# Performance work log

Hardware: AMD Instinct MI355X
Metric: run time of the kernel (lower is better)

## Reference

```python
import jax, jax.numpy as jnp
import numpy as np

E = 8          # num experts
TOPK = 2
D = 1024       # emb_size (expert hidden == emb_size)


def setup_inputs() -> dict:
    key = jax.random.key(0)
    ks = jax.random.split(key, 8)
    s = 1.0 / np.sqrt(D)
    x = jax.random.normal(ks[0], (4, 1024, D), dtype=jnp.float32)
    gate_W = jax.random.uniform(ks[1], (E, D), jnp.float32, -s, s)   # torch Linear weight (out,in)
    gate_b = jax.random.uniform(ks[2], (E,), jnp.float32, -s, s)
    w1 = jax.random.uniform(ks[3], (E, D, D), jnp.float32, -s, s)    # per-expert first Linear (out,in)
    b1 = jax.random.uniform(ks[4], (E, D), jnp.float32, -s, s)
    w2 = jax.random.uniform(ks[5], (E, D, D), jnp.float32, -s, s)    # per-expert second Linear (out,in)
    b2 = jax.random.uniform(ks[6], (E, D), jnp.float32, -s, s)
    return {"x": x, "gate_W": gate_W, "gate_b": gate_b,
            "w1": w1, "b1": b1, "w2": w2, "b2": b2}


def reference(x, gate_W, gate_b, w1, b1, w2, b2):
    x_shape = x.shape
    xt = x.reshape(-1, x_shape[-1])                       # [N, D]

    # gating
    gate_logits = xt @ gate_W.T + gate_b                  # [N, E]
    gate_prob = jax.nn.softmax(gate_logits, axis=-1)      # [N, E]
    top_w, top_i = jax.lax.top_k(gate_prob, TOPK)         # [N, K]
    top_w = jax.nn.softmax(top_w, axis=-1)                # renormalize over top-k

    # dense per-expert MLP: h = relu(x @ W1^T + b1); o = h @ W2^T + b2
    h = jax.nn.relu(jnp.einsum('nd,ehd->neh', xt, w1) + b1[None])   # [N, E, D]
    o = jnp.einsum('neh,eoh->neo', h, w2) + b2[None]                # [N, E, D]

    # gather top-k expert outputs per token and combine with weights
    o_top = jnp.take_along_axis(o, top_i[:, :, None], axis=1)       # [N, K, D]
    y = jnp.sum(o_top * top_w[:, :, None], axis=1)                  # [N, D]

    return y.reshape(x_shape), gate_prob
```

## Files before the change

kernel.cpp:

```cpp
#include <hip/hip_runtime.h>

#define NTOK 4096
#define DIM 1024
#define NE 8
#define NPAIR (NTOK * 2)

typedef __bf16 bf16x8 __attribute__((ext_vector_type(8)));
typedef float floatx4 __attribute__((ext_vector_type(4)));

__device__ __forceinline__ unsigned short f2bf(float f) {
  unsigned u = __float_as_uint(f);
  u = u + 0x7fffu + ((u >> 16) & 1u);
  return (unsigned short)(u >> 16);
}
__device__ __forceinline__ float bf2f(unsigned short h) {
  return __uint_as_float(((unsigned)h) << 16);
}

__device__ __forceinline__ void gld_lds16(const unsigned short* g, unsigned short* l) {
  __builtin_amdgcn_global_load_lds(
      (const __attribute__((address_space(1))) void*)g,
      (__attribute__((address_space(3))) void*)l, 16, 0, 0);
}

__global__ __launch_bounds__(256) void gate_kernel(
    const float* __restrict__ x, const float* __restrict__ gW,
    const float* __restrict__ gb,
    float* __restrict__ gp_out, int2* __restrict__ tops,
    float* __restrict__ pairw, int* __restrict__ cnt, int* __restrict__ done,
    unsigned short* __restrict__ x_bf)
{
  const int tid = threadIdx.x;
  if (blockIdx.x == 0) {
    if (tid < NE) cnt[tid] = 0;
    if (tid == NE) *done = 0;
  }
  const int lane = tid & 63;
  const int wid = tid >> 6;
  const int t = blockIdx.x * 4 + wid;

  float4 xv[4];
#pragma unroll
  for (int j = 0; j < 4; j++)
    xv[j] = ((const float4*)(x + (size_t)t * DIM))[lane + 64 * j];

#pragma unroll
  for (int j = 0; j < 4; j++) {
    ushort4 o;
    o.x = f2bf(xv[j].x); o.y = f2bf(xv[j].y);
    o.z = f2bf(xv[j].z); o.w = f2bf(xv[j].w);
    ((ushort4*)(x_bf + (size_t)t * DIM))[lane + 64 * j] = o;
  }

  float p[NE];
#pragma unroll
  for (int e = 0; e < NE; e++) {
    const float4* gwe = (const float4*)(gW + e * DIM);
    float s = 0.f;
#pragma unroll
    for (int j = 0; j < 4; j++) {
      float4 g = gwe[lane + 64 * j];
      s += xv[j].x * g.x + xv[j].y * g.y + xv[j].z * g.z + xv[j].w * g.w;
    }
    p[e] = s;
  }
#pragma unroll
  for (int e = 0; e < NE; e++) {
#pragma unroll
    for (int off = 32; off >= 1; off >>= 1) p[e] += __shfl_xor(p[e], off);
  }

  float m = -1e30f;
#pragma unroll
  for (int e = 0; e < NE; e++) { p[e] += gb[e]; m = fmaxf(m, p[e]); }
  float s = 0.f;
  float pr[NE];
#pragma unroll
  for (int e = 0; e < NE; e++) { pr[e] = __expf(p[e] - m); s += pr[e]; }
  float inv = 1.f / s;
#pragma unroll
  for (int e = 0; e < NE; e++) pr[e] *= inv;

  if (lane < NE) gp_out[(size_t)t * NE + lane] = pr[lane];

  if (lane == 0) {
    int i0 = 0;
#pragma unroll
    for (int e = 1; e < NE; e++) if (pr[e] > pr[i0]) i0 = e;
    int i1 = (i0 == 0) ? 1 : 0;
#pragma unroll
    for (int e = 0; e < NE; e++) if (e != i0 && pr[e] > pr[i1]) i1 = e;
    float d = __expf(pr[i1] - pr[i0]);
    float w0 = 1.f / (1.f + d);
    tops[t] = make_int2(i0, i1);
    pairw[t * 2] = w0;
    pairw[t * 2 + 1] = 1.f - w0;
  }
}

__global__ __launch_bounds__(256) void bin_sched_kernel(
    const int2* __restrict__ tops, int* __restrict__ cnt,
    int* __restrict__ bucket,
    int* __restrict__ posmap,
    int* __restrict__ done, int* __restrict__ base,
    int* __restrict__ sched, int* __restrict__ sched_n)
{
  const int t = blockIdx.x * 256 + threadIdx.x;
  const int lane = threadIdx.x & 63;
  int2 ti = tops[t];
#pragma unroll
  for (int slot = 0; slot < 2; slot++) {
    int e = slot ? ti.y : ti.x;
#pragma unroll
    for (int ex = 0; ex < NE; ex++) {
      bool mine = (e == ex);
      unsigned long long mask = __ballot(mine);
      if (mask) {
        int leader = __ffsll((long long)mask) - 1;
        int total = __popcll(mask);
        int prefix = __popcll(mask & ((1ull << lane) - 1ull));
        int idx = 0;
        if (lane == leader) idx = atomicAdd(&cnt[ex], total);
        idx = __shfl(idx, leader) + prefix;
        if (mine) {
          bucket[ex * NTOK + idx] = t * 2 + slot;
          posmap[t * 2 + slot] = (ex << 16) | idx;
        }
      }
    }
  }
  __syncthreads();
  if (threadIdx.x == 0) {
    if (atomicAdd(done, 1) == gridDim.x - 1) {
      int b = 0, pos = 0;
      for (int e = 0; e < NE; e++) {
        int c = atomicAdd(&cnt[e], 0);
        base[e] = b;
        int tiles = (c + 127) >> 7;
        for (int i = 0; i < tiles; i++) {
          int valid = c - i * 128; if (valid > 128) valid = 128;
          sched[pos++] = (e << 20) | (i << 8) | valid;
        }
        b += c;
      }
      base[NE] = b;
      *sched_n = pos;
    }
  }
}

__global__ __launch_bounds__(256) void cvt_kernel(
    const float4* __restrict__ src, ushort4* __restrict__ dst)
{
  const int i = blockIdx.x * 256 + threadIdx.x;
  float4 v = src[i];
  ushort4 o;
  o.x = f2bf(v.x); o.y = f2bf(v.y); o.z = f2bf(v.z); o.w = f2bf(v.w);
  dst[i] = o;
}

template <int RELU, int GATHER>
__global__ __launch_bounds__(256) void ffn_gemm(
    const unsigned short* __restrict__ A,
    const unsigned short* __restrict__ B,
    const float* __restrict__ bias,
    const int* __restrict__ base,
    const int* __restrict__ bucket,
    const int* __restrict__ sched, const int* __restrict__ sched_n,
    unsigned short* __restrict__ Out)
{
  const int l = blockIdx.x;
  const int xcd = l & 7;
  const int w = l >> 3;
  const int nt = w & 7;
  const int slot = xcd * 9 + (w >> 3);
  if (slot >= *sched_n) return;
  const int se = sched[slot];
  const int e = se >> 20;
  const int mt = (se >> 8) & 0xfff;
  const int valid = se & 255;
  const int arow0 = base[e] + mt * 128;

  __shared__ unsigned short lda[2][128 * 64];
  __shared__ unsigned short ldb[2][128 * 64];

  const int tid = threadIdx.x;
  const int lane = tid & 63;
  const int wid = tid >> 6;

  const unsigned short* ap[4];
  const unsigned short* bp[4];
#pragma unroll
  for (int j = 0; j < 4; j++) {
    int g = wid * 4 + j;
    int row = g * 8 + (lane >> 3);
    int gran = (lane & 7) ^ (row & 7);
    if (GATHER) {
      int idx = mt * 128 + row;
      int ce = base[e + 1] - base[e];
      if (idx > ce - 1) idx = ce - 1;
      int tok = bucket[e * NTOK + idx] >> 1;
      ap[j] = A + (size_t)tok * DIM + (gran << 3);
    } else {
      int prow = arow0 + row;
      if (prow > NPAIR - 1) prow = NPAIR - 1;
      ap[j] = A + (size_t)prow * DIM + (gran << 3);
    }
    bp[j] = B + ((size_t)e * DIM + nt * 128 + row) * DIM + (gran << 3);
  }

  floatx4 acc[4][4] = {};
  const int wm = (wid & 1) * 64;
  const int wn = (wid >> 1) * 64;
  const int quad = lane >> 4;
  const int cl = lane & 15;
  const int sw = cl & 7;

  auto stage = [&](int b) {
#pragma unroll
    for (int j = 0; j < 4; j++) {
      int g = wid * 4 + j;
      gld_lds16(ap[j], &lda[b][g * 512]);
      gld_lds16(bp[j], &ldb[b][g * 512]);
      ap[j] += 64;
      bp[j] += 64;
    }
  };
  auto compute = [&](int b) {
    const unsigned short* la = lda[b];
    const unsigned short* lb = ldb[b];
#pragma unroll
    for (int kk = 0; kk < 64; kk += 32) {
      const int gb = (kk >> 3) + quad;
      const int goff = ((gb ^ sw) << 3);
      bf16x8 af[4], bfr[4];
#pragma unroll
      for (int mi = 0; mi < 4; mi++)
        af[mi] = *(const bf16x8*)&la[(wm + mi * 16 + cl) * 64 + goff];
#pragma unroll
      for (int ni = 0; ni < 4; ni++)
        bfr[ni] = *(const bf16x8*)&lb[(wn + ni * 16 + cl) * 64 + goff];
#pragma unroll
      for (int mi = 0; mi < 4; mi++)
#pragma unroll
        for (int ni = 0; ni < 4; ni++)
          acc[mi][ni] = __builtin_amdgcn_mfma_f32_16x16x32_bf16(af[mi], bfr[ni], acc[mi][ni], 0, 0, 0);
    }
  };

  stage(0);
  asm volatile("s_waitcnt vmcnt(0)" ::: "memory");
  __builtin_amdgcn_s_barrier();

#pragma unroll 1
  for (int i = 0; i < 7; i++) {
    stage(1);
    compute(0);
    asm volatile("s_waitcnt vmcnt(0)" ::: "memory");
    __builtin_amdgcn_s_barrier();
    stage(0);
    compute(1);
    asm volatile("s_waitcnt vmcnt(0)" ::: "memory");
    __builtin_amdgcn_s_barrier();
  }
  stage(1);
  compute(0);
  asm volatile("s_waitcnt vmcnt(0)" ::: "memory");
  __builtin_amdgcn_s_barrier();
  compute(1);

#pragma unroll
  for (int ni = 0; ni < 4; ni++) {
    int col = nt * 128 + wn + ni * 16 + cl;
    float bval = bias[e * DIM + col];
#pragma unroll
    for (int mi = 0; mi < 4; mi++) {
#pragma unroll
      for (int reg = 0; reg < 4; reg++) {
        int rl = wm + mi * 16 + quad * 4 + reg;
        if (rl < valid) {
          float v = acc[mi][ni][reg] + bval;
          if (RELU) v = fmaxf(v, 0.f);
          Out[(size_t)(arow0 + rl) * DIM + col] = f2bf(v);
        }
      }
    }
  }
}

__global__ __launch_bounds__(256) void combine_kernel(
    const unsigned short* __restrict__ o, const int* __restrict__ posmap,
    const int* __restrict__ base, const float* __restrict__ pairw,
    float* __restrict__ y)
{
  const int t = blockIdx.x;
  const int tid = threadIdx.x;
  const int pm0 = posmap[t * 2], pm1 = posmap[t * 2 + 1];
  const int p0 = base[pm0 >> 16] + (pm0 & 0xffff);
  const int p1 = base[pm1 >> 16] + (pm1 & 0xffff);
  const float w0 = pairw[t * 2], w1 = pairw[t * 2 + 1];
  ushort4 a = ((const ushort4*)(o + (size_t)p0 * DIM))[tid];
  ushort4 b = ((const ushort4*)(o + (size_t)p1 * DIM))[tid];
  float4 r;
  r.x = w0 * bf2f(a.x) + w1 * bf2f(b.x);
  r.y = w0 * bf2f(a.y) + w1 * bf2f(b.y);
  r.z = w0 * bf2f(a.z) + w1 * bf2f(b.z);
  r.w = w0 * bf2f(a.w) + w1 * bf2f(b.w);
  ((float4*)(y + (size_t)t * DIM))[tid] = r;
}

extern "C" void kernel_launch(void* const* d_in, const int* in_sizes, int n_in,
                              void* d_out, int out_size, void* d_ws, size_t ws_size,
                              hipStream_t stream) {
  const float* x  = (const float*)d_in[0];
  const float* gW = (const float*)d_in[1];
  const float* gb = (const float*)d_in[2];
  const float* w1 = (const float*)d_in[3];
  const float* b1 = (const float*)d_in[4];
  const float* w2 = (const float*)d_in[5];
  const float* b2 = (const float*)d_in[6];
  float* y  = (float*)d_out;
  float* gp = (float*)d_out + (size_t)NTOK * DIM;

  char* ws = (char*)d_ws;
  unsigned short* x_bf   = (unsigned short*)(ws);
  unsigned short* w2_bf  = (unsigned short*)(ws);
  unsigned short* h_pack = (unsigned short*)(ws + (size_t)(16u << 20));
  unsigned short* w1_bf  = (unsigned short*)(ws + (size_t)(32u << 20));
  unsigned short* o_pack = (unsigned short*)(ws + (size_t)(32u << 20));
  char* tail = ws + (size_t)(48u << 20);
  int*   cnt     = (int*)(tail);
  int*   done    = cnt + NE;
  int*   base    = done + 1;
  int*   sched   = base + NE + 1;
  int*   sched_n = sched + 128;
  int*   bucket  = sched_n + 1;
  float* pairw   = (float*)(bucket + NE * NTOK);
  int2*  tops    = (int2*)(pairw + NPAIR);
  int*   posmap  = (int*)(tops + NTOK);

  const int cvt_blocks = (NE * DIM * DIM / 4) / 256;
  gate_kernel<<<NTOK / 4, 256, 0, stream>>>(x, gW, gb, gp, tops, pairw, cnt, done, x_bf);
  bin_sched_kernel<<<NTOK / 256, 256, 0, stream>>>(tops, cnt, bucket, posmap, done,
                                                   base, sched, sched_n);
  cvt_kernel<<<cvt_blocks, 256, 0, stream>>>((const float4*)w1, (ushort4*)w1_bf);
  ffn_gemm<1, 1><<<576, 256, 0, stream>>>(x_bf, w1_bf, b1, base, bucket, sched, sched_n, h_pack);
  cvt_kernel<<<cvt_blocks, 256, 0, stream>>>((const float4*)w2, (ushort4*)w2_bf);
  ffn_gemm<0, 0><<<576, 256, 0, stream>>>(h_pack, w2_bf, b2, base, bucket, sched, sched_n, o_pack);
  combine_kernel<<<NTOK, 256, 0, stream>>>(o_pack, posmap, base, pairw, y);
}
```

Before: 264.0 us.

## Halve expert GEMM M-tile to 64 rows and use single-buffered LDS

The expert schedule now uses 64-row token tiles instead of 128, and the grid grows so that 17 slots per XCD cover the larger tile count. Each of the four waves now handles a 64x32 slice of output. The double-buffered LDS staging is replaced by a single buffer with a barrier on each K step. The aim is better load balance across CUs for uneven expert sizes and higher occupancy from the smaller LDS footprint. In exchange, loads no longer overlap compute, and each block re-reads the full weight tile for fewer rows, which doubles weight traffic per token.

```diff
diff --git a/kernel.cpp b/kernel.cpp
--- a/kernel.cpp
+++ b/kernel.cpp
@@ -4,6 +4,7 @@
 #define DIM 1024
 #define NE 8
 #define NPAIR (NTOK * 2)
+#define NSLOT 17
 
 typedef __bf16 bf16x8 __attribute__((ext_vector_type(8)));
 typedef float floatx4 __attribute__((ext_vector_type(4)));
@@ -136,9 +137,9 @@
       for (int e = 0; e < NE; e++) {
         int c = atomicAdd(&cnt[e], 0);
         base[e] = b;
-        int tiles = (c + 127) >> 7;
+        int tiles = (c + 63) >> 6;
         for (int i = 0; i < tiles; i++) {
-          int valid = c - i * 128; if (valid > 128) valid = 128;
+          int valid = c - i * 64; if (valid > 64) valid = 64;
           sched[pos++] = (e << 20) | (i << 8) | valid;
         }
         b += c;
@@ -173,30 +174,30 @@
   const int xcd = l & 7;
   const int w = l >> 3;
   const int nt = w & 7;
-  const int slot = xcd * 9 + (w >> 3);
+  const int slot = xcd * NSLOT + (w >> 3);
   if (slot >= *sched_n) return;
   const int se = sched[slot];
   const int e = se >> 20;
   const int mt = (se >> 8) & 0xfff;
   const int valid = se & 255;
-  const int arow0 = base[e] + mt * 128;
-
-  __shared__ unsigned short lda[2][128 * 64];
-  __shared__ unsigned short ldb[2][128 * 64];
+  const int arow0 = base[e] + mt * 64;
+
+  __shared__ unsigned short lda[64 * 64];
+  __shared__ unsigned short ldb[128 * 64];
 
   const int tid = threadIdx.x;
   const int lane = tid & 63;
   const int wid = tid >> 6;
 
-  const unsigned short* ap[4];
+  const unsigned short* ap[2];
   const unsigned short* bp[4];
 #pragma unroll
-  for (int j = 0; j < 4; j++) {
-    int g = wid * 4 + j;
+  for (int j = 0; j < 2; j++) {
+    int g = wid * 2 + j;
     int row = g * 8 + (lane >> 3);
     int gran = (lane & 7) ^ (row & 7);
     if (GATHER) {
-      int idx = mt * 128 + row;
+      int idx = mt * 64 + row;
       int ce = base[e + 1] - base[e];
       if (idx > ce - 1) idx = ce - 1;
       int tok = bucket[e * NTOK + idx] >> 1;
@@ -206,78 +207,62 @@
       if (prow > NPAIR - 1) prow = NPAIR - 1;
       ap[j] = A + (size_t)prow * DIM + (gran << 3);
     }
+  }
+#pragma unroll
+  for (int j = 0; j < 4; j++) {
+    int g = wid * 4 + j;
+    int row = g * 8 + (lane >> 3);
+    int gran = (lane & 7) ^ (row & 7);
     bp[j] = B + ((size_t)e * DIM + nt * 128 + row) * DIM + (gran << 3);
   }
 
-  floatx4 acc[4][4] = {};
-  const int wm = (wid & 1) * 64;
-  const int wn = (wid >> 1) * 64;
+  floatx4 acc[4][2] = {};
+  const int wn = wid * 32;
   const int quad = lane >> 4;
   const int cl = lane & 15;
   const int sw = cl & 7;
 
-  auto stage = [&](int b) {
+  for (int k0 = 0; k0 < 16; k0++) {
+#pragma unroll
+    for (int j = 0; j < 2; j++) {
+      gld_lds16(ap[j], &lda[(wid * 2 + j) * 512]);
+      ap[j] += 64;
+    }
 #pragma unroll
     for (int j = 0; j < 4; j++) {
-      int g = wid * 4 + j;
-      gld_lds16(ap[j], &lda[b][g * 512]);
-      gld_lds16(bp[j], &ldb[b][g * 512]);
-      ap[j] += 64;
+      gld_lds16(bp[j], &ldb[(wid * 4 + j) * 512]);
       bp[j] += 64;
     }
-  };
-  auto compute = [&](int b) {
-    const unsigned short* la = lda[b];
-    const unsigned short* lb = ldb[b];
+    __syncthreads();
 #pragma unroll
     for (int kk = 0; kk < 64; kk += 32) {
       const int gb = (kk >> 3) + quad;
       const int goff = ((gb ^ sw) << 3);
-      bf16x8 af[4], bfr[4];
+      bf16x8 af[4], bfr[2];
 #pragma unroll
       for (int mi = 0; mi < 4; mi++)
-        af[mi] = *(const bf16x8*)&la[(wm + mi * 16 + cl) * 64 + goff];
-#pragma unroll
-      for (int ni = 0; ni < 4; ni++)
-        bfr[ni] = *(const bf16x8*)&lb[(wn + ni * 16 + cl) * 64 + goff];
+        af[mi] = *(const bf16x8*)&lda[(mi * 16 + cl) * 64 + goff];
+#pragma unroll
+      for (int ni = 0; ni < 2; ni++)
+        bfr[ni] = *(const bf16x8*)&ldb[(wn + ni * 16 + cl) * 64 + goff];
 #pragma unroll
       for (int mi = 0; mi < 4; mi++)
 #pragma unroll
-        for (int ni = 0; ni < 4; ni++)
+        for (int ni = 0; ni < 2; ni++)
           acc[mi][ni] = __builtin_amdgcn_mfma_f32_16x16x32_bf16(af[mi], bfr[ni], acc[mi][ni], 0, 0, 0);
     }
-  };
-
-  stage(0);
-  asm volatile("s_waitcnt vmcnt(0)" ::: "memory");
-  __builtin_amdgcn_s_barrier();
-
-#pragma unroll 1
-  for (int i = 0; i < 7; i++) {
-    stage(1);
-    compute(0);
-    asm volatile("s_waitcnt vmcnt(0)" ::: "memory");
-    __builtin_amdgcn_s_barrier();
-    stage(0);
-    compute(1);
-    asm volatile("s_waitcnt vmcnt(0)" ::: "memory");
-    __builtin_amdgcn_s_barrier();
-  }
-  stage(1);
-  compute(0);
-  asm volatile("s_waitcnt vmcnt(0)" ::: "memory");
-  __builtin_amdgcn_s_barrier();
-  compute(1);
-
-#pragma unroll
-  for (int ni = 0; ni < 4; ni++) {
+    if (k0 < 15) __syncthreads();
+  }
+
+#pragma unroll
+  for (int ni = 0; ni < 2; ni++) {
     int col = nt * 128 + wn + ni * 16 + cl;
     float bval = bias[e * DIM + col];
 #pragma unroll
     for (int mi = 0; mi < 4; mi++) {
 #pragma unroll
       for (int reg = 0; reg < 4; reg++) {
-        int rl = wm + mi * 16 + quad * 4 + reg;
+        int rl = mi * 16 + quad * 4 + reg;
         if (rl < valid) {
           float v = acc[mi][ni][reg] + bval;
           if (RELU) v = fmaxf(v, 0.f);
@@ -333,19 +318,20 @@
   int*   done    = cnt + NE;
   int*   base    = done + 1;
   int*   sched   = base + NE + 1;
-  int*   sched_n = sched + 128;
+  int*   sched_n = sched + 256;
   int*   bucket  = sched_n + 1;
   float* pairw   = (float*)(bucket + NE * NTOK);
   int2*  tops    = (int2*)(pairw + NPAIR);
   int*   posmap  = (int*)(tops + NTOK);
 
   const int cvt_blocks = (NE * DIM * DIM / 4) / 256;
+  const int gemm_grid = 8 * NSLOT * 8;
   gate_kernel<<<NTOK / 4, 256, 0, stream>>>(x, gW, gb, gp, tops, pairw, cnt, done, x_bf);
   bin_sched_kernel<<<NTOK / 256, 256, 0, stream>>>(tops, cnt, bucket, posmap, done,
                                                    base, sched, sched_n);
   cvt_kernel<<<cvt_blocks, 256, 0, stream>>>((const float4*)w1, (ushort4*)w1_bf);
-  ffn_gemm<1, 1><<<576, 256, 0, stream>>>(x_bf, w1_bf, b1, base, bucket, sched, sched_n, h_pack);
+  ffn_gemm<1, 1><<<gemm_grid, 256, 0, stream>>>(x_bf, w1_bf, b1, base, bucket, sched, sched_n, h_pack);
   cvt_kernel<<<cvt_blocks, 256, 0, stream>>>((const float4*)w2, (ushort4*)w2_bf);
-  ffn_gemm<0, 0><<<576, 256, 0, stream>>>(h_pack, w2_bf, b2, base, bucket, sched, sched_n, o_pack);
+  ffn_gemm<0, 0><<<gemm_grid, 256, 0, stream>>>(h_pack, w2_bf, b2, base, bucket, sched, sched_n, o_pack);
   combine_kernel<<<NTOK, 256, 0, stream>>>(o_pack, posmap, base, pairw, y);
 }
```

Measured after the change: 233.5 us. -11.5%, faster.

## Halve GEMM K-tile to 32 with new LDS swizzle and partial vmcnt pipelining

Applied to the files above, without the earlier changes.

Shrinks the per-stage K slice in the expert GEMM from 64 to 32, halving the LDS footprint, and changes the XOR swizzle to fit 32-wide rows with precomputed LDS offsets. The main loop now issues the next stage's loads and waits with vmcnt(4), so the next tile's loads stay in flight while the current tile is computed, rather than draining all loads every iteration. This gives more barriers per K and less MFMA work per barrier, in exchange for better load/compute overlap and possibly higher occupancy from the smaller LDS use. The sched_n offset also moves from 128 to 256 in the workspace layout.

```diff
diff --git a/kernel.cpp b/kernel.cpp
--- a/kernel.cpp
+++ b/kernel.cpp
@@ -181,32 +181,32 @@
   const int valid = se & 255;
   const int arow0 = base[e] + mt * 128;
 
-  __shared__ unsigned short lda[2][128 * 64];
-  __shared__ unsigned short ldb[2][128 * 64];
+  __shared__ unsigned short lda[2][128 * 32];
+  __shared__ unsigned short ldb[2][128 * 32];
 
   const int tid = threadIdx.x;
   const int lane = tid & 63;
   const int wid = tid >> 6;
 
-  const unsigned short* ap[4];
-  const unsigned short* bp[4];
-#pragma unroll
-  for (int j = 0; j < 4; j++) {
-    int g = wid * 4 + j;
-    int row = g * 8 + (lane >> 3);
-    int gran = (lane & 7) ^ (row & 7);
+  const unsigned short* aps[2];
+  const unsigned short* bps[2];
+#pragma unroll
+  for (int j = 0; j < 2; j++) {
+    int G = wid * 128 + j * 64 + lane;
+    int r = G >> 2;
+    int g = (G & 3) ^ ((r >> 1) & 3);
     if (GATHER) {
-      int idx = mt * 128 + row;
+      int idx = mt * 128 + r;
       int ce = base[e + 1] - base[e];
       if (idx > ce - 1) idx = ce - 1;
       int tok = bucket[e * NTOK + idx] >> 1;
-      ap[j] = A + (size_t)tok * DIM + (gran << 3);
+      aps[j] = A + (size_t)tok * DIM + g * 8;
     } else {
-      int prow = arow0 + row;
+      int prow = arow0 + r;
       if (prow > NPAIR - 1) prow = NPAIR - 1;
-      ap[j] = A + (size_t)prow * DIM + (gran << 3);
-    }
-    bp[j] = B + ((size_t)e * DIM + nt * 128 + row) * DIM + (gran << 3);
+      aps[j] = A + (size_t)prow * DIM + g * 8;
+    }
+    bps[j] = B + ((size_t)e * DIM + nt * 128 + r) * DIM + g * 8;
   }
 
   floatx4 acc[4][4] = {};
@@ -214,57 +214,53 @@
   const int wn = (wid >> 1) * 64;
   const int quad = lane >> 4;
   const int cl = lane & 15;
-  const int sw = cl & 7;
+
+  int offA[4], offB[4];
+#pragma unroll
+  for (int i = 0; i < 4; i++) {
+    int m = wm + i * 16 + cl;
+    offA[i] = m * 32 + ((quad ^ ((m >> 1) & 3)) << 3);
+    int n = wn + i * 16 + cl;
+    offB[i] = n * 32 + ((quad ^ ((n >> 1) & 3)) << 3);
+  }
 
   auto stage = [&](int b) {
 #pragma unroll
-    for (int j = 0; j < 4; j++) {
-      int g = wid * 4 + j;
-      gld_lds16(ap[j], &lda[b][g * 512]);
-      gld_lds16(bp[j], &ldb[b][g * 512]);
-      ap[j] += 64;
-      bp[j] += 64;
+    for (int j = 0; j < 2; j++) {
+      gld_lds16(aps[j], &lda[b][(wid * 2 + j) * 512]);
+      aps[j] += 32;
+    }
+#pragma unroll
+    for (int j = 0; j < 2; j++) {
+      gld_lds16(bps[j], &ldb[b][(wid * 2 + j) * 512]);
+      bps[j] += 32;
     }
   };
   auto compute = [&](int b) {
     const unsigned short* la = lda[b];
     const unsigned short* lb = ldb[b];
-#pragma unroll
-    for (int kk = 0; kk < 64; kk += 32) {
-      const int gb = (kk >> 3) + quad;
-      const int goff = ((gb ^ sw) << 3);
-      bf16x8 af[4], bfr[4];
-#pragma unroll
-      for (int mi = 0; mi < 4; mi++)
-        af[mi] = *(const bf16x8*)&la[(wm + mi * 16 + cl) * 64 + goff];
+    bf16x8 af[4], bfr[4];
+#pragma unroll
+    for (int mi = 0; mi < 4; mi++) af[mi] = *(const bf16x8*)&la[offA[mi]];
+#pragma unroll
+    for (int ni = 0; ni < 4; ni++) bfr[ni] = *(const bf16x8*)&lb[offB[ni]];
+#pragma unroll
+    for (int mi = 0; mi < 4; mi++)
 #pragma unroll
       for (int ni = 0; ni < 4; ni++)
-        bfr[ni] = *(const bf16x8*)&lb[(wn + ni * 16 + cl) * 64 + goff];
-#pragma unroll
-      for (int mi = 0; mi < 4; mi++)
-#pragma unroll
-        for (int ni = 0; ni < 4; ni++)
-          acc[mi][ni] = __builtin_amdgcn_mfma_f32_16x16x32_bf16(af[mi], bfr[ni], acc[mi][ni], 0, 0, 0);
-    }
+        acc[mi][ni] = __builtin_amdgcn_mfma_f32_16x16x32_bf16(af[mi], bfr[ni], acc[mi][ni], 0, 0, 0);
   };
 
   stage(0);
-  asm volatile("s_waitcnt vmcnt(0)" ::: "memory");
-  __builtin_amdgcn_s_barrier();
 
 #pragma unroll 1
-  for (int i = 0; i < 7; i++) {
-    stage(1);
-    compute(0);
-    asm volatile("s_waitcnt vmcnt(0)" ::: "memory");
+  for (int t = 0; t < 31; ++t) {
+    stage((t + 1) & 1);
+    asm volatile("s_waitcnt vmcnt(4)" ::: "memory");
     __builtin_amdgcn_s_barrier();
-    stage(0);
-    compute(1);
-    asm volatile("s_waitcnt vmcnt(0)" ::: "memory");
+    compute(t & 1);
     __builtin_amdgcn_s_barrier();
   }
-  stage(1);
-  compute(0);
   asm volatile("s_waitcnt vmcnt(0)" ::: "memory");
   __builtin_amdgcn_s_barrier();
   compute(1);
@@ -333,19 +329,20 @@
   int*   done    = cnt + NE;
   int*   base    = done + 1;
   int*   sched   = base + NE + 1;
-  int*   sched_n = sched + 128;
+  int*   sched_n = sched + 256;
   int*   bucket  = sched_n + 1;
   float* pairw   = (float*)(bucket + NE * NTOK);
   int2*  tops    = (int2*)(pairw + NPAIR);
   int*   posmap  = (int*)(tops + NTOK);
 
   const int cvt_blocks = (NE * DIM * DIM / 4) / 256;
+  const int gemm_grid = 576;
   gate_kernel<<<NTOK / 4, 256, 0, stream>>>(x, gW, gb, gp, tops, pairw, cnt, done, x_bf);
   bin_sched_kernel<<<NTOK / 256, 256, 0, stream>>>(tops, cnt, bucket, posmap, done,
                                                    base, sched, sched_n);
   cvt_kernel<<<cvt_blocks, 256, 0, stream>>>((const float4*)w1, (ushort4*)w1_bf);
-  ffn_gemm<1, 1><<<576, 256, 0, stream>>>(x_bf, w1_bf, b1, base, bucket, sched, sched_n, h_pack);
+  ffn_gemm<1, 1><<<gemm_grid, 256, 0, stream>>>(x_bf, w1_bf, b1, base, bucket, sched, sched_n, h_pack);
   cvt_kernel<<<cvt_blocks, 256, 0, stream>>>((const float4*)w2, (ushort4*)w2_bf);
-  ffn_gemm<0, 0><<<576, 256, 0, stream>>>(h_pack, w2_bf, b2, base, bucket, sched, sched_n, o_pack);
+  ffn_gemm<0, 0><<<gemm_grid, 256, 0, stream>>>(h_pack, w2_bf, b2, base, bucket, sched, sched_n, o_pack);
   combine_kernel<<<NTOK, 256, 0, stream>>>(o_pack, posmap, base, pairw, y);
 }
```

New measurement: 247.8 us. 6.1% less time.
